# Kernel optimization log

Hardware: AMD Instinct MI355X
Metric: run time of the kernel (lower is better)

## Reference

```python
import jax, jax.numpy as jnp
import numpy as np

B, N, C = 8, 4096, 768
H, HD = 12, 64          # num_heads, head_dim = C // H
M = HD * 2              # rand_feat_dim
LAM = 0.3
NUM_STEP = 5


def setup_inputs() -> dict:
    key = jax.random.key(0)
    k1, k2, k3, k4 = jax.random.split(key, 4)
    x = jax.random.normal(k1, (B, N, C), dtype=jnp.float32)
    Wqkv = jax.random.normal(k2, (C, 2 * C), dtype=jnp.float32) * 0.02
    Wproj = jax.random.normal(k3, (C, C), dtype=jnp.float32) * 0.02
    bproj = jnp.zeros((C,), dtype=jnp.float32)
    rand_matrix = jax.random.normal(k4, (H, HD, M), dtype=jnp.float32)
    return {"x": x, "Wqkv": Wqkv, "Wproj": Wproj, "bproj": bproj,
            "rand_matrix": rand_matrix}


def _soft(z, t):
    # sign(z) * relu(|z| - t): soft-thresholding (ISTA proximal step)
    return jnp.sign(z) * jax.nn.relu(jnp.abs(z) - t)


def reference(x, Wqkv, Wproj, bproj, rand_matrix):
    Bn, Nn, Cn = x.shape
    Hh, hd, m = rand_matrix.shape
    scale = hd ** (-0.5)

    qkv = x @ Wqkv                                   # [B,N,2C]
    q = qkv[..., :Cn].reshape(Bn, Nn, Hh, hd).transpose(0, 2, 1, 3)  # [B,H,N,hd]
    v = qkv[..., Cn:].reshape(Bn, Nn, Hh, hd).transpose(0, 2, 1, 3)  # [B,H,N,hd]

    # random-feature map: exp(q @ proj - ||q||^2 / 2) / sqrt(m)
    qs = q * scale ** 0.5
    rf = jnp.exp(jnp.einsum('bhnd,hdm->bhnm', qs, rand_matrix)
                 - 0.5 * jnp.sum(qs * qs, axis=-1, keepdims=True)) / m ** 0.5
    # F.normalize(p=2, dim=-2): normalize over the sequence axis
    qn = rf / jnp.maximum(jnp.linalg.norm(rf, axis=-2, keepdims=True), 1e-12)

    kk = jnp.einsum('bhnm,bhnp->bhmp', qn, qn)       # [B,H,m,m]
    kv = jnp.einsum('bhnm,bhnd->bhmd', qn, v)        # [B,H,m,hd]

    # Lipschitz bound: max row L1 norm of kk, detached
    L = jax.lax.stop_gradient(
        jnp.max(jnp.sum(jnp.abs(kk), axis=-1), axis=-1))[..., None, None] + 1.0

    # unrolled ISTA soft-thresholding loop
    s = _soft(kv, LAM)
    for _ in range(NUM_STEP):
        s = _soft(s - (kk @ s - kv) / L, LAM / L)

    out = jnp.einsum('bhnm,bhmd->bhnd', qn, s)       # [B,H,N,hd]
    out = out.transpose(0, 2, 1, 3).reshape(Bn, Nn, Cn)
    return out @ Wproj + bproj
```

## Files before the change

kernel.cpp:

```cpp
#include <hip/hip_runtime.h>


typedef __attribute__((ext_vector_type(8))) short bf16x8;
typedef __attribute__((ext_vector_type(4))) float f32x4;

#define GLD16(gptr, lptr)                                                              \
  __builtin_amdgcn_global_load_lds((const __attribute__((address_space(1))) void*)(gptr), \
                                   (__attribute__((address_space(3))) void*)(lptr), 16, 0, 0)

__device__ __forceinline__ unsigned short f2bf(float f) {
  union { float f; unsigned int u; } v; v.f = f;
  unsigned int r = v.u + 0x7fffu + ((v.u >> 16) & 1u);
  return (unsigned short)(r >> 16);
}
__device__ __forceinline__ float bf2f(unsigned short s) {
  union { unsigned int u; float f; } v; v.u = ((unsigned int)s) << 16;
  return v.f;
}
__device__ __forceinline__ float rn_of(float css) {
  return 1.f / fmaxf(sqrtf(css), 1e-12f);
}

template<int ITERS>
__device__ __forceinline__ void gemm256_core(
    const unsigned short* __restrict__ A,
    const unsigned short* __restrict__ B,
    int ldk,
    f32x4 (&acc)[8][4],
    unsigned short* smem) {
  const int tid = threadIdx.x;
  const int lane = tid & 63, wave = tid >> 6;
  const int l16 = lane & 15, quad = lane >> 4;
  const int wr = wave >> 2, wc = wave & 3;
  const int rsw = l16 & 7;

#pragma unroll
  for (int i = 0; i < 8; i++)
#pragma unroll
    for (int j = 0; j < 4; j++)
#pragma unroll
      for (int r = 0; r < 4; r++) acc[i][j][r] = 0.f;

  const int srow0 = tid >> 3, sc0 = ((tid & 7) ^ (srow0 & 7)) << 3;
  const int srow1 = (tid + 512) >> 3, sc1 = ((tid & 7) ^ (srow1 & 7)) << 3;
  const int dstw = wave * 512;

  auto stageA = [&](int T, int h) {
    const unsigned short* g = A + (long)(h * 128) * ldk + T * 64;
    unsigned short* d = smem + (T & 1) * 32768 + h * 8192 + dstw;
    GLD16(g + (long)srow0 * ldk + sc0, d);
    GLD16(g + (long)srow1 * ldk + sc1, d + 4096);
  };
  auto stageB = [&](int T, int h) {
    const unsigned short* g = B + (long)(h * 128) * ldk + T * 64;
    unsigned short* d = smem + (T & 1) * 32768 + 16384 + h * 8192 + dstw;
    GLD16(g + (long)srow0 * ldk + sc0, d);
    GLD16(g + (long)srow1 * ldk + sc1, d + 4096);
  };

  bf16x8 af[4][2], bn[4][2];

  auto rdA_ks = [&](int b, int mh, int ks) {
    const unsigned short* p = smem + b * 32768 + wr * 8192 + (mh * 64 + l16) * 64;
#pragma unroll
    for (int ii = 0; ii < 4; ii++)
      af[ii][ks] = *(const bf16x8*)(p + ii * 1024 + (((ks * 4 + quad) ^ rsw) << 3));
  };
  auto rdB_ks = [&](int b, int ks) {
    const unsigned short* p = smem + b * 32768 + 16384 + (wc >> 1) * 8192 +
                              ((wc & 1) * 64 + l16) * 64;
#pragma unroll
    for (int jj = 0; jj < 4; jj++)
      bn[jj][ks] = *(const bf16x8*)(p + jj * 1024 + (((ks * 4 + quad) ^ rsw) << 3));
  };

  auto mma16 = [&](int mh, int ks) {
    __builtin_amdgcn_s_setprio(1);
#pragma unroll
    for (int ii = 0; ii < 4; ii++)
#pragma unroll
      for (int jj = 0; jj < 4; jj++)
        acc[mh * 4 + ii][jj] = __builtin_amdgcn_mfma_f32_16x16x32_bf16(
            af[ii][ks], bn[jj][ks], acc[mh * 4 + ii][jj], 0, 0, 0);
    __builtin_amdgcn_s_setprio(0);
  };

#define FENCE asm volatile("" ::: "memory")
#define SGB __builtin_amdgcn_sched_barrier(0)
#define LGKM(n) asm volatile("s_waitcnt lgkmcnt(" #n ")" ::: "memory")

  stageA(0, 0); stageA(0, 1); stageB(0, 0); stageB(0, 1);
  stageB(1, 0); stageB(1, 1);
  asm volatile("s_waitcnt vmcnt(4)" ::: "memory");
  __builtin_amdgcn_s_barrier();

#pragma unroll 1
  for (int i = 0; i < ITERS; i++) {
    const int u = 2 * i;
    const bool more = (i + 1 < ITERS);
    stageA(u + 1, 0);
    rdB_ks(0, 0); rdA_ks(0, 0, 0);
    SGB;
    rdB_ks(0, 1); rdA_ks(0, 0, 1);
    FENCE; __builtin_amdgcn_s_barrier();
    LGKM(8); SGB;
    mma16(0, 0);
    LGKM(0); SGB;
    mma16(0, 1);
    FENCE; __builtin_amdgcn_s_barrier();
    stageA(u + 1, 1);
    if (more) stageB(u + 2, 0);
    rdA_ks(0, 1, 0);
    SGB;
    rdA_ks(0, 1, 1);
    FENCE; __builtin_amdgcn_s_barrier();
    LGKM(4); SGB;
    mma16(1, 0);
    LGKM(0); SGB;
    mma16(1, 1);
    if (more) { asm volatile("s_waitcnt vmcnt(2)" ::: "memory"); }
    else      { asm volatile("s_waitcnt vmcnt(0)" ::: "memory"); }
    FENCE; __builtin_amdgcn_s_barrier();
    if (more) { stageB(u + 2, 1); stageA(u + 2, 0); stageA(u + 2, 1); }
    rdB_ks(1, 0); rdA_ks(1, 0, 0);
    SGB;
    rdB_ks(1, 1); rdA_ks(1, 0, 1);
    FENCE; __builtin_amdgcn_s_barrier();
    LGKM(8); SGB;
    mma16(0, 0);
    LGKM(0); SGB;
    mma16(0, 1);
    FENCE; __builtin_amdgcn_s_barrier();
    if (more) { stageB(u + 3, 0); stageB(u + 3, 1); }
    rdA_ks(1, 1, 0);
    SGB;
    rdA_ks(1, 1, 1);
    FENCE; __builtin_amdgcn_s_barrier();
    LGKM(4); SGB;
    mma16(1, 0);
    LGKM(0); SGB;
    mma16(1, 1);
    if (more) { asm volatile("s_waitcnt vmcnt(4)" ::: "memory"); }
    FENCE; __builtin_amdgcn_s_barrier();
  }
#undef FENCE
#undef SGB
#undef LGKM
}

template<int NT>
__device__ __forceinline__ void gemm128x256_core(
    const unsigned short* __restrict__ A,
    const unsigned short* __restrict__ B,
    int ldk,
    f32x4 (&acc)[4][4],
    unsigned short* smem) {
  const int tid = threadIdx.x;
  const int lane = tid & 63, wave = tid >> 6;
  const int l16 = lane & 15, quad = lane >> 4;
  const int wr = wave >> 2, wc = wave & 3;
  const int rsw = l16 & 7;

#pragma unroll
  for (int m = 0; m < 4; m++)
#pragma unroll
    for (int n = 0; n < 4; n++)
#pragma unroll
      for (int r = 0; r < 4; r++) acc[m][n][r] = 0.f;

  const int srow0 = tid >> 3, sc0 = ((tid & 7) ^ (srow0 & 7)) << 3;
  const int srow1 = (tid + 512) >> 3, sc1 = ((tid & 7) ^ (srow1 & 7)) << 3;
  const int dstw = wave * 512;

  auto stage = [&](int T) {
    unsigned short* d = smem + (T & 1) * 24576;
    const unsigned short* gA = A + T * 64;
    const unsigned short* gB = B + T * 64;
    GLD16(gA + (long)srow0 * ldk + sc0, d + dstw);
    GLD16(gA + (long)srow1 * ldk + sc1, d + 4096 + dstw);
    GLD16(gB + (long)srow0 * ldk + sc0, d + 8192 + dstw);
    GLD16(gB + (long)srow1 * ldk + sc1, d + 8192 + 4096 + dstw);
    GLD16(gB + (long)(srow0 + 128) * ldk + sc0, d + 16384 + dstw);
    GLD16(gB + (long)(srow1 + 128) * ldk + sc1, d + 16384 + 4096 + dstw);
  };

  bf16x8 af[4][2], bn[4][2];

  auto rdA_ks = [&](int b, int ks) {
    const unsigned short* p = smem + b * 24576 + (wr * 64 + l16) * 64;
#pragma unroll
    for (int m = 0; m < 4; m++)
      af[m][ks] = *(const bf16x8*)(p + m * 1024 + (((ks * 4 + quad) ^ rsw) << 3));
  };
  auto rdB_ks = [&](int b, int ks) {
    const unsigned short* p = smem + b * 24576 + 8192 + (wc * 64 + l16) * 64;
#pragma unroll
    for (int n = 0; n < 4; n++)
      bn[n][ks] = *(const bf16x8*)(p + n * 1024 + (((ks * 4 + quad) ^ rsw) << 3));
  };

  auto mma16 = [&](int ks) {
    __builtin_amdgcn_s_setprio(1);
#pragma unroll
    for (int m = 0; m < 4; m++)
#pragma unroll
      for (int n = 0; n < 4; n++)
        acc[m][n] = __builtin_amdgcn_mfma_f32_16x16x32_bf16(
            af[m][ks], bn[n][ks], acc[m][n], 0, 0, 0);
    __builtin_amdgcn_s_setprio(0);
  };

#define FENCE asm volatile("" ::: "memory")
#define SGB __builtin_amdgcn_sched_barrier(0)
#define LGKM(n) asm volatile("s_waitcnt lgkmcnt(" #n ")" ::: "memory")

  stage(0); stage(1);
  asm volatile("s_waitcnt vmcnt(6)" ::: "memory");
  __builtin_amdgcn_s_barrier();

#pragma unroll 1
  for (int t = 0; t < NT; t++) {
    const int b = t & 1;
    rdA_ks(b, 0); rdB_ks(b, 0);
    SGB;
    rdA_ks(b, 1); rdB_ks(b, 1);
    LGKM(8); SGB;
    mma16(0);
    LGKM(0); SGB;
    mma16(1);
    FENCE; __builtin_amdgcn_s_barrier();
    if (t + 2 < NT) stage(t + 2);
    if (t + 1 < NT) {
      if (t + 2 < NT) { asm volatile("s_waitcnt vmcnt(6)" ::: "memory"); }
      else            { asm volatile("s_waitcnt vmcnt(0)" ::: "memory"); }
      FENCE; __builtin_amdgcn_s_barrier();
    }
  }
#undef FENCE
#undef SGB
#undef LGKM
}

__global__ __launch_bounds__(256) void k_convert_bf16(const float* __restrict__ in,
                                                      unsigned short* __restrict__ out, long n4) {
  long i = (long)blockIdx.x * 256 + threadIdx.x;
  if (i < n4) {
    float4 v = ((const float4*)in)[i];
    unsigned short o[4] = {f2bf(v.x), f2bf(v.y), f2bf(v.z), f2bf(v.w)};
    ((uint2*)out)[i] = *(uint2*)o;
  }
}

__global__ __launch_bounds__(256) void k_transpose_tiled(const float* __restrict__ in,
                                                         unsigned short* __restrict__ out,
                                                         int R, int C, float scale) {
  __shared__ float t[32][33];
  const float* ib = in + (long)blockIdx.z * R * C;
  unsigned short* ob = out + (long)blockIdx.z * R * C;
  int c0 = blockIdx.x * 32, r0 = blockIdx.y * 32;
  int tx = threadIdx.x & 31, ty = threadIdx.x >> 5;
#pragma unroll
  for (int k = 0; k < 32; k += 8)
    t[ty + k][tx] = ib[(long)(r0 + ty + k) * C + c0 + tx];
  __syncthreads();
#pragma unroll
  for (int k = 0; k < 32; k += 8)
    ob[(long)(c0 + ty + k) * R + r0 + tx] = f2bf(t[tx][ty + k] * scale);
}

__global__ __launch_bounds__(512, 2) void k_gemm_qkv256(const unsigned short* __restrict__ xbf,
                                                        const unsigned short* __restrict__ wqkvT,
                                                        unsigned short* __restrict__ q,
                                                        unsigned short* __restrict__ vT) {
  __shared__ __align__(16) unsigned short smem[65536];
  f32x4 acc[8][4];
  const int L = blockIdx.x;
  const int xcd = L & 7, slot = L >> 3;
  const int rt = xcd * 16 + slot / 6;
  const int ct = slot % 6;
  gemm256_core<6>(xbf + (long)rt * 256 * 768, wqkvT + (long)ct * 256 * 768, 768, acc, smem);

  const int tid = threadIdx.x, lane = tid & 63, wave = tid >> 6;
  const int l16 = lane & 15, quad = lane >> 4;
  const int wr = wave >> 2, wc = wave & 3;
  const int b = rt >> 4;
  const int nbase = (rt & 15) * 256;
  if (ct < 3) {
#pragma unroll
    for (int i = 0; i < 8; i++)
#pragma unroll
      for (int j = 0; j < 4; j++) {
        int col = ct * 256 + wc * 64 + j * 16 + l16;
        int h = col >> 6, d = col & 63;
#pragma unroll
        for (int r = 0; r < 4; r++) {
          int n = nbase + wr * 128 + i * 16 + quad * 4 + r;
          q[((long)(b * 12 + h) * 4096 + n) * 64 + d] = f2bf(acc[i][j][r]);
        }
      }
  } else {
    unsigned short* pool = smem;
    for (int hh = 0; hh < 2; hh++) {
      __syncthreads();
      if (wr == hh) {
#pragma unroll
        for (int i = 0; i < 8; i++)
#pragma unroll
          for (int j = 0; j < 4; j++)
#pragma unroll
            for (int r = 0; r < 4; r++)
              pool[(wc * 64 + j * 16 + l16) * 136 + i * 16 + quad * 4 + r] = f2bf(acc[i][j][r]);
      }
      __syncthreads();
#pragma unroll
      for (int it = 0; it < 8; it++) {
        int chunk = it * 512 + tid;
        int col = chunk >> 4, ng = chunk & 15;
        uint4 val = *(const uint4*)&pool[col * 136 + ng * 8];
        int vcol = (ct - 3) * 256 + col;
        int h = vcol >> 6, d = vcol & 63;
        long n = nbase + hh * 128 + ng * 8;
        *(uint4*)&vT[((long)(b * 12 + h) * 64 + d) * 4096 + n] = val;
      }
    }
  }
}

__global__ __launch_bounds__(256) void k_gemm_rf(const unsigned short* __restrict__ q,
                                                 const unsigned short* __restrict__ rmT,
                                                 unsigned short* __restrict__ qnT,
                                                 float* __restrict__ colss) {
  __shared__ __align__(16) unsigned short smem[16384];
  __shared__ float hnp[256];
  __shared__ float css[128];
  unsigned short* Asm = smem;
  unsigned short* Bsm = smem + 8192;
  unsigned short* pool = smem;
  f32x4 acc[4][4];
  const int nt = blockIdx.x, bh = blockIdx.y, h = bh % 12;
  const int tid = threadIdx.x, lane = tid & 63, wave = tid >> 6;
  const int l16 = lane & 15, quad = lane >> 4;
  const int wm = (wave >> 1) * 64, wn = (wave & 1) * 64;
  const int fsw = (l16 >> 1) & 3;
  const unsigned short* Aq = q + ((long)bh * 4096 + nt * 128) * 64;
  const unsigned short* Brm = rmT + (long)h * 8192;

#pragma unroll
  for (int c = 0; c < 4; c++) {
    int chunk = c * 256 + tid;
    int row = chunk >> 3, ko8 = chunk & 7;
    int kc = ko8 >> 2;
    int c2s = (ko8 & 3) ^ ((row >> 1) & 3);
    *(uint4*)(Asm + kc * 4096 + row * 32 + c2s * 8) = *(const uint4*)(Aq + (long)row * 64 + ko8 * 8);
    *(uint4*)(Bsm + kc * 4096 + row * 32 + c2s * 8) = *(const uint4*)(Brm + (long)row * 64 + ko8 * 8);
  }
  for (int i = tid; i < 128; i += 256) css[i] = 0.f;
  __syncthreads();
  {
    const unsigned short* ap = Asm + (tid & 1) * 4096 + (tid >> 1) * 32;
    float ssum = 0.f;
#pragma unroll
    for (int e = 0; e < 32; e++) { float f = bf2f(ap[e]); ssum += f * f; }
    hnp[tid] = ssum;
  }
#pragma unroll
  for (int i = 0; i < 4; i++)
#pragma unroll
    for (int j = 0; j < 4; j++)
#pragma unroll
      for (int r = 0; r < 4; r++) acc[i][j][r] = 0.f;
#pragma unroll
  for (int kc = 0; kc < 2; kc++) {
    bf16x8 af[4], bfr[4];
#pragma unroll
    for (int i = 0; i < 4; i++)
      af[i] = *(const bf16x8*)(Asm + kc * 4096 + (wm + i * 16 + l16) * 32 + ((quad ^ fsw) * 8));
#pragma unroll
    for (int j = 0; j < 4; j++)
      bfr[j] = *(const bf16x8*)(Bsm + kc * 4096 + (wn + j * 16 + l16) * 32 + ((quad ^ fsw) * 8));
#pragma unroll
    for (int i = 0; i < 4; i++)
#pragma unroll
      for (int j = 0; j < 4; j++)
        acc[i][j] = __builtin_amdgcn_mfma_f32_16x16x32_bf16(af[i], bfr[j], acc[i][j], 0, 0, 0);
  }
  __syncthreads();
  float hnv[4][4];
#pragma unroll
  for (int i = 0; i < 4; i++)
#pragma unroll
    for (int r = 0; r < 4; r++) {
      int row = wm + i * 16 + quad * 4 + r;
      hnv[i][r] = 0.0625f * (hnp[2 * row] + hnp[2 * row + 1]);
    }
#pragma unroll
  for (int j = 0; j < 4; j++) {
    int col = wn + j * 16 + l16;
    float cp = 0.f;
#pragma unroll
    for (int i = 0; i < 4; i++)
#pragma unroll
      for (int r = 0; r < 4; r++) {
        float v = __expf(acc[i][j][r] - hnv[i][r]) * 0.08838834764831845f;
        acc[i][j][r] = v;
        cp += v * v;
      }
    atomicAdd(&css[col], cp);
  }
  __syncthreads();
  for (int i = tid; i < 128; i += 256) atomicAdd(&colss[bh * 128 + i], css[i]);
  for (int hh = 0; hh < 2; hh++) {
    __syncthreads();
    if ((wave >> 1) == hh) {
#pragma unroll
      for (int i = 0; i < 4; i++)
#pragma unroll
        for (int j = 0; j < 4; j++)
#pragma unroll
          for (int r = 0; r < 4; r++)
            pool[(i * 16 + quad * 4 + r) * 134 + wn + j * 16 + l16] = f2bf(acc[i][j][r]);
    }
    __syncthreads();
#pragma unroll
    for (int c = 0; c < 4; c++) {
      int chunk = tid + c * 256;
      int m = chunk >> 3, nj = (chunk & 7) * 8;
      unsigned short o[8];
#pragma unroll
      for (int e = 0; e < 8; e++) o[e] = pool[(nj + e) * 134 + m];
      *(uint4*)&qnT[((long)bh * 128 + m) * 4096 + nt * 128 + hh * 64 + nj] = *(uint4*)o;
    }
  }
}

__global__ __launch_bounds__(256) void k_gemm_kkkv(const unsigned short* __restrict__ qnT,
                                                   const unsigned short* __restrict__ vT,
                                                   const float* __restrict__ colss,
                                                   unsigned short* __restrict__ kkp) {
  __shared__ __align__(16) unsigned short As[128 * 32], Bs[64 * 32];
  f32x4 acc[4][6];
  const int ks = blockIdx.x, bh = blockIdx.y;
  const unsigned short* A = qnT + (long)bh * 128 * 4096 + ks * 512;
  const unsigned short* B1 = vT + (long)bh * 64 * 4096 + ks * 512;
  const int tid = threadIdx.x, lane = tid & 63, wave = tid >> 6;
  const int l16 = lane & 15, quad = lane >> 4;
  const int wm = (wave >> 1) * 64, wn = (wave & 1) * 96;
  const int arow = tid >> 2;
  const int akos = (((tid & 3) ^ ((arow >> 1) & 3)) << 3);
  const int fsw = (l16 >> 1) & 3;
#pragma unroll
  for (int i = 0; i < 4; i++)
#pragma unroll
    for (int j = 0; j < 6; j++)
#pragma unroll
      for (int r = 0; r < 4; r++) acc[i][j][r] = 0.f;
  for (int k0 = 0; k0 < 512; k0 += 32) {
    __syncthreads();
    GLD16(A + (long)arow * 4096 + k0 + akos, As + wave * 512);
    GLD16(A + (long)(arow + 64) * 4096 + k0 + akos, As + 2048 + wave * 512);
    GLD16(B1 + (long)arow * 4096 + k0 + akos, Bs + wave * 512);
    __syncthreads();
    bf16x8 af[4], bfr[6];
#pragma unroll
    for (int i = 0; i < 4; i++)
      af[i] = *(const bf16x8*)(As + (wm + i * 16 + l16) * 32 + ((quad ^ fsw) * 8));
#pragma unroll
    for (int j = 0; j < 6; j++) {
      int row = wn + j * 16 + l16;
      const unsigned short* rp = (row < 128) ? (As + row * 32) : (Bs + (row - 128) * 32);
      bfr[j] = *(const bf16x8*)(rp + ((quad ^ fsw) * 8));
    }
#pragma unroll
    for (int i = 0; i < 4; i++)
#pragma unroll
      for (int j = 0; j < 6; j++)
        acc[i][j] = __builtin_amdgcn_mfma_f32_16x16x32_bf16(af[i], bfr[j], acc[i][j], 0, 0, 0);
  }
  unsigned short* dst = kkp + ((long)ks * 96 + bh) * 24576;
  float rnr[4][4];
#pragma unroll
  for (int i = 0; i < 4; i++)
#pragma unroll
    for (int r = 0; r < 4; r++)
      rnr[i][r] = rn_of(colss[bh * 128 + wm + i * 16 + quad * 4 + r]);
#pragma unroll
  for (int j = 0; j < 6; j++) {
    int col = wn + j * 16 + l16;
    float rnc = (col < 128) ? rn_of(colss[bh * 128 + col]) : 1.f;
#pragma unroll
    for (int i = 0; i < 4; i++)
#pragma unroll
      for (int r = 0; r < 4; r++) {
        int row = wm + i * 16 + quad * 4 + r;
        dst[row * 192 + col] = f2bf(acc[i][j][r] * rnr[i][r] * rnc);
      }
  }
}

__global__ __launch_bounds__(256) void k_red(const unsigned short* __restrict__ kkp,
                                             unsigned short* __restrict__ kkred,
                                             float* __restrict__ kvred) {
  const int g = blockIdx.x, bh = blockIdx.y;
  const int tid = threadIdx.x;
  const unsigned short* base = kkp + (long)bh * 24576 + (long)(g * 32) * 192;
#pragma unroll
  for (int c = 0; c < 3; c++) {
    int idx = c * 256 + tid;
    int m = idx / 24, c8 = idx % 24;
    float f[8] = {0.f, 0.f, 0.f, 0.f, 0.f, 0.f, 0.f, 0.f};
#pragma unroll
    for (int ks = 0; ks < 8; ks++) {
      union { uint4 u; unsigned short s[8]; } u;
      u.u = *(const uint4*)(base + (long)ks * 2359296 + m * 192 + c8 * 8);
#pragma unroll
      for (int e = 0; e < 8; e++) f[e] += bf2f(u.s[e]);
    }
    long row = (long)bh * 128 + g * 32 + m;
    if (c8 < 16) {
      unsigned short o[8];
#pragma unroll
      for (int e = 0; e < 8; e++) o[e] = f2bf(f[e]);
      *(uint4*)&kkred[row * 128 + c8 * 8] = *(uint4*)o;
    } else {
      *(float4*)&kvred[row * 64 + (c8 - 16) * 8] = make_float4(f[0], f[1], f[2], f[3]);
      *(float4*)&kvred[row * 64 + (c8 - 16) * 8 + 4] = make_float4(f[4], f[5], f[6], f[7]);
    }
  }
}

__global__ __launch_bounds__(256) void k_ista2(const unsigned short* __restrict__ kkred,
                                               const float* __restrict__ kvred,
                                               const float* __restrict__ colss,
                                               unsigned short* __restrict__ sT) {
  __shared__ __align__(16) unsigned short kks[128 * 144];
  __shared__ __align__(16) unsigned short ssT[64 * 144];
  __shared__ float kvs[128 * 64];
  __shared__ float red[128];
  __shared__ float rns[128];
  const int tid = threadIdx.x, lane = tid & 63, wave = tid >> 6;
  const int l16 = lane & 15, quad = lane >> 4;
  const int wm = (wave >> 1) * 64, wn = (wave & 1) * 32;
  const int bh = blockIdx.x;
  for (int idx = tid; idx < 2048; idx += 256) {
    int m = idx >> 4, c8 = idx & 15;
    uint4 v = *(const uint4*)(kkred + ((long)bh * 128 + m) * 128 + c8 * 8);
    *(uint4*)&kks[m * 144 + c8 * 8] = v;
  }
  for (int idx = tid; idx < 2048; idx += 256) {
    int m = idx >> 4, c4 = idx & 15;
    float4 v = *(const float4*)(kvred + ((long)bh * 128 + m) * 64 + c4 * 4);
    *(float4*)&kvs[m * 64 + c4 * 4] = v;
  }
  __syncthreads();
  float kv[4][2][4];
#pragma unroll
  for (int i = 0; i < 4; i++)
#pragma unroll
    for (int j = 0; j < 2; j++)
#pragma unroll
      for (int r = 0; r < 4; r++) {
        int m = wm + i * 16 + quad * 4 + r, d = wn + j * 16 + l16;
        kv[i][j][r] = kvs[m * 64 + d];
      }
  if (tid < 128) {
    float rs = 0.f;
    const unsigned short* rp = kks + tid * 144;
    for (int p = 0; p < 128; p++) rs += fabsf(bf2f(rp[p]));
    red[tid] = rs;
    rns[tid] = rn_of(colss[bh * 128 + tid]);
  }
  __syncthreads();
  for (int o = 64; o > 0; o >>= 1) {
    if (tid < o) red[tid] = fmaxf(red[tid], red[tid + o]);
    __syncthreads();
  }
  const float L = red[0] + 1.f;
  const float invL = 1.f / L;
  const float lamL = 0.3f * invL;
  float sreg[4][2][4];
#pragma unroll
  for (int i = 0; i < 4; i++)
#pragma unroll
    for (int j = 0; j < 2; j++)
#pragma unroll
      for (int r = 0; r < 4; r++) {
        float z = kv[i][j][r];
        float az = fabsf(z) - 0.3f;
        float s = az > 0.f ? copysignf(az, z) : 0.f;
        sreg[i][j][r] = s;
        ssT[(wn + j * 16 + l16) * 144 + wm + i * 16 + quad * 4 + r] = f2bf(s);
      }
  for (int step = 0; step < 5; step++) {
    __syncthreads();
    f32x4 acc[4][2];
#pragma unroll
    for (int i = 0; i < 4; i++)
#pragma unroll
      for (int j = 0; j < 2; j++)
#pragma unroll
        for (int r = 0; r < 4; r++) acc[i][j][r] = 0.f;
#pragma unroll
    for (int kc = 0; kc < 4; kc++) {
      bf16x8 af[4], bfj[2];
#pragma unroll
      for (int i = 0; i < 4; i++)
        af[i] = *(const bf16x8*)(kks + (wm + i * 16 + l16) * 144 + kc * 32 + quad * 8);
#pragma unroll
      for (int j = 0; j < 2; j++)
        bfj[j] = *(const bf16x8*)(ssT + (wn + j * 16 + l16) * 144 + kc * 32 + quad * 8);
#pragma unroll
      for (int i = 0; i < 4; i++)
#pragma unroll
        for (int j = 0; j < 2; j++)
          acc[i][j] = __builtin_amdgcn_mfma_f32_16x16x32_bf16(af[i], bfj[j], acc[i][j], 0, 0, 0);
    }
    __syncthreads();
#pragma unroll
    for (int i = 0; i < 4; i++)
#pragma unroll
      for (int j = 0; j < 2; j++)
#pragma unroll
        for (int r = 0; r < 4; r++) {
          float z = sreg[i][j][r] - (acc[i][j][r] - kv[i][j][r]) * invL;
          float az = fabsf(z) - lamL;
          float s = az > 0.f ? copysignf(az, z) : 0.f;
          sreg[i][j][r] = s;
          ssT[(wn + j * 16 + l16) * 144 + wm + i * 16 + quad * 4 + r] = f2bf(s);
        }
  }
#pragma unroll
  for (int i = 0; i < 4; i++)
#pragma unroll
    for (int j = 0; j < 2; j++)
#pragma unroll
      for (int r = 0; r < 4; r++) {
        int m = wm + i * 16 + quad * 4 + r, d = wn + j * 16 + l16;
        sT[(long)bh * 8192 + d * 128 + m] = f2bf(sreg[i][j][r] * rns[m]);
      }
}

__global__ __launch_bounds__(256) void k_gemm_attn(const unsigned short* __restrict__ qnT,
                                                   const unsigned short* __restrict__ sT,
                                                   unsigned short* __restrict__ attn) {
  __shared__ __align__(16) unsigned short As2[4352];
  __shared__ __align__(16) unsigned short Bs[64 * 32];
  f32x4 acc[4][2];
  const int nt = blockIdx.x, bh = blockIdx.y;
  const int b = bh / 12, h = bh % 12;
  const int tid = threadIdx.x, lane = tid & 63, wave = tid >> 6;
  const int l16 = lane & 15, quad = lane >> 4;
  const int wm = (wave >> 1) * 64, wn = (wave & 1) * 32;
  const int fsw = (l16 >> 1) & 3;
#pragma unroll
  for (int i = 0; i < 4; i++)
#pragma unroll
    for (int j = 0; j < 2; j++)
#pragma unroll
      for (int r = 0; r < 4; r++) acc[i][j][r] = 0.f;
  for (int k0 = 0; k0 < 128; k0 += 32) {
    __syncthreads();
#pragma unroll
    for (int it = 0; it < 3; it++) {
      if (it < 2 || tid < 32) {
        int c = it * 256 + tid;
        int p = (c * 241) >> 12;
        int nh = c - p * 17;
        int k = ((p & 7) << 2) + (p >> 3);
        int n8 = (nh < 16 ? nh : 15) << 3;
        const unsigned short* gp = qnT + ((long)bh * 128 + k0 + k) * 4096 + nt * 128 + n8;
        GLD16(gp, As2 + (it * 256 + wave * 64) * 8);
      }
    }
    {
      int dd = tid >> 2;
      int ko = (((tid & 3) ^ ((dd >> 1) & 3)) * 8);
      const unsigned short* gp = sT + ((long)bh * 64 + dd) * 128 + k0 + ko;
      GLD16(gp, Bs + wave * 512);
    }
    __syncthreads();
    bf16x8 af[4], bfr[2];
#pragma unroll
    for (int i = 0; i < 4; i++) {
      union { bf16x8 v; unsigned short s[8]; } u;
#pragma unroll
      for (int e = 0; e < 8; e++) {
        int p = ((e & 3) << 3) + (quad << 1) + (e >> 2);
        u.s[e] = As2[p * 136 + wm + i * 16 + l16];
      }
      af[i] = u.v;
    }
#pragma unroll
    for (int j = 0; j < 2; j++)
      bfr[j] = *(const bf16x8*)&Bs[(wn + j * 16 + l16) * 32 + ((quad ^ fsw) * 8)];
#pragma unroll
    for (int i = 0; i < 4; i++)
#pragma unroll
      for (int j = 0; j < 2; j++)
        acc[i][j] = __builtin_amdgcn_mfma_f32_16x16x32_bf16(af[i], bfr[j], acc[i][j], 0, 0, 0);
  }
#pragma unroll
  for (int i = 0; i < 4; i++)
#pragma unroll
    for (int j = 0; j < 2; j++)
#pragma unroll
      for (int r = 0; r < 4; r++) {
        int n = nt * 128 + wm + i * 16 + quad * 4 + r;
        int dd = wn + j * 16 + l16;
        attn[((long)b * 4096 + n) * 768 + h * 64 + dd] = f2bf(acc[i][j][r]);
      }
}

__global__ __launch_bounds__(512, 2) void k_gemm_proj128(const unsigned short* __restrict__ attn,
                                                         const unsigned short* __restrict__ wprojT,
                                                         const float* __restrict__ bias,
                                                         float* __restrict__ out) {
  __shared__ __align__(16) unsigned short smem[49152];
  f32x4 acc[4][4];
  const int L = blockIdx.x;
  const int xcd = L & 7, slot = L >> 3;
  const int rt = xcd * 32 + slot / 3;
  const int ct = slot % 3;
  gemm128x256_core<12>(attn + (long)rt * 128 * 768, wprojT + (long)ct * 256 * 768, 768,
                       acc, smem);
  const int tid = threadIdx.x, lane = tid & 63, wave = tid >> 6;
  const int l16 = lane & 15, quad = lane >> 4;
  const int wr = wave >> 2, wc = wave & 3;
  const long row0 = (long)rt * 128 + wr * 64;
#pragma unroll
  for (int m = 0; m < 4; m++)
#pragma unroll
    for (int n = 0; n < 4; n++) {
      int col = ct * 256 + wc * 64 + n * 16 + l16;
      float bv = bias[col];
#pragma unroll
      for (int r = 0; r < 4; r++) {
        long row = row0 + m * 16 + quad * 4 + r;
        out[row * 768 + col] = acc[m][n][r] + bv;
      }
    }
}

extern "C" void kernel_launch(void* const* d_in, const int* in_sizes, int n_in,
                              void* d_out, int out_size, void* d_ws, size_t ws_size,
                              hipStream_t stream) {
  const float* x = (const float*)d_in[0];
  const float* Wqkv = (const float*)d_in[1];
  const float* Wproj = (const float*)d_in[2];
  const float* bproj = (const float*)d_in[3];
  const float* rm = (const float*)d_in[4];
  float* out = (float*)d_out;

  size_t o = 0;
  char* wsb = (char*)d_ws;
  auto take = [&](size_t b) { char* p = wsb + o; o += b; return p; };
  unsigned short* wqkvT = (unsigned short*)take(2359296);
  unsigned short* wprojT = (unsigned short*)take(1179648);
  unsigned short* rmT = (unsigned short*)take(196608);
  unsigned short* q = (unsigned short*)take(50331648);
  unsigned short* vT = (unsigned short*)take(50331648);
  float* colss = (float*)take(49152);
  unsigned short* sT = (unsigned short*)take(1572864);
  if (ws_size < o) return;

  unsigned short* xbf = (unsigned short*)d_out;
  unsigned short* qnT = (unsigned short*)d_out;
  unsigned short* kkp = q;
  unsigned short* attnbf = q;
  unsigned short* kkred = vT;
  float* kvred = (float*)(vT + 1572864);

  hipMemsetAsync(colss, 0, 49152, stream);

  k_convert_bf16<<<24576, 256, 0, stream>>>(x, xbf, 6291456L);
  k_transpose_tiled<<<dim3(48, 24, 1), 256, 0, stream>>>(Wqkv, wqkvT, 768, 1536, 1.0f);
  k_transpose_tiled<<<dim3(24, 24, 1), 256, 0, stream>>>(Wproj, wprojT, 768, 768, 1.0f);
  k_transpose_tiled<<<dim3(4, 2, 12), 256, 0, stream>>>(rm, rmT, 64, 128, 0.3535533905932738f);
  k_gemm_qkv256<<<768, 512, 0, stream>>>(xbf, wqkvT, q, vT);
  k_gemm_rf<<<dim3(32, 96), 256, 0, stream>>>(q, rmT, qnT, colss);
  k_gemm_kkkv<<<dim3(8, 96), 256, 0, stream>>>(qnT, vT, colss, kkp);
  k_red<<<dim3(4, 96), 256, 0, stream>>>(kkp, kkred, kvred);
  k_ista2<<<96, 256, 0, stream>>>(kkred, kvred, colss, sT);
  k_gemm_attn<<<dim3(32, 96), 256, 0, stream>>>(qnT, sT, attnbf);
  k_gemm_proj128<<<768, 512, 0, stream>>>(attnbf, wprojT, bproj, out);
}
```

Measured before the change: 450.5 us.

## Merge preprocessing launches into one kernel and split ISTA across head-dim halves

Folds the bf16 conversion of x, the three weight transposes and the colss zeroing into a single k_pre launch, replacing one memset and four separate launches. It also splits the ISTA kernel so each block handles 32 of the 64 head-dim columns, doubling the grid from 96 to 192 blocks. The intent is to cut launch and serialization overhead and to occupy more CUs in the small ISTA stage. The cost is that kk is loaded and its Lipschitz reduction recomputed redundantly in both halves.

```diff
diff --git a/kernel.cpp b/kernel.cpp
--- a/kernel.cpp
+++ b/kernel.cpp
@@ -241,31 +241,53 @@
 #undef LGKM
 }
 
-__global__ __launch_bounds__(256) void k_convert_bf16(const float* __restrict__ in,
-                                                      unsigned short* __restrict__ out, long n4) {
-  long i = (long)blockIdx.x * 256 + threadIdx.x;
-  if (i < n4) {
-    float4 v = ((const float4*)in)[i];
+__global__ __launch_bounds__(256) void k_pre(const float* __restrict__ x,
+                                             unsigned short* __restrict__ xbf,
+                                             const float* __restrict__ Wqkv,
+                                             unsigned short* __restrict__ wqkvT,
+                                             const float* __restrict__ Wproj,
+                                             unsigned short* __restrict__ wprojT,
+                                             const float* __restrict__ rm,
+                                             unsigned short* __restrict__ rmT,
+                                             float* __restrict__ colss) {
+  __shared__ float t[32][33];
+  const int bid = blockIdx.x, tid = threadIdx.x;
+  if (bid < 24576) {
+    long i = (long)bid * 256 + tid;
+    float4 v = ((const float4*)x)[i];
     unsigned short o[4] = {f2bf(v.x), f2bf(v.y), f2bf(v.z), f2bf(v.w)};
-    ((uint2*)out)[i] = *(uint2*)o;
-  }
-}
-
-__global__ __launch_bounds__(256) void k_transpose_tiled(const float* __restrict__ in,
-                                                         unsigned short* __restrict__ out,
-                                                         int R, int C, float scale) {
-  __shared__ float t[32][33];
-  const float* ib = in + (long)blockIdx.z * R * C;
-  unsigned short* ob = out + (long)blockIdx.z * R * C;
-  int c0 = blockIdx.x * 32, r0 = blockIdx.y * 32;
-  int tx = threadIdx.x & 31, ty = threadIdx.x >> 5;
+    ((uint2*)xbf)[i] = *(uint2*)o;
+    return;
+  }
+  int b2 = bid - 24576;
+  const float* in; unsigned short* out; int R, C, c0, r0; float scale;
+  if (b2 < 1152) {
+    in = Wqkv; out = wqkvT; R = 768; C = 1536;
+    c0 = (b2 % 48) * 32; r0 = (b2 / 48) * 32; scale = 1.f;
+  } else if (b2 < 1152 + 576) {
+    b2 -= 1152;
+    in = Wproj; out = wprojT; R = 768; C = 768;
+    c0 = (b2 % 24) * 32; r0 = (b2 / 24) * 32; scale = 1.f;
+  } else if (b2 < 1152 + 576 + 96) {
+    b2 -= 1152 + 576;
+    int z = b2 / 8;
+    in = rm + (long)z * 8192; out = rmT + (long)z * 8192;
+    R = 64; C = 128;
+    c0 = (b2 % 4) * 32; r0 = ((b2 / 4) & 1) * 32;
+    scale = 0.3535533905932738f;
+  } else {
+    b2 -= 1152 + 576 + 96;
+    colss[b2 * 256 + tid] = 0.f;
+    return;
+  }
+  int tx = tid & 31, ty = tid >> 5;
 #pragma unroll
   for (int k = 0; k < 32; k += 8)
-    t[ty + k][tx] = ib[(long)(r0 + ty + k) * C + c0 + tx];
+    t[ty + k][tx] = in[(long)(r0 + ty + k) * C + c0 + tx];
   __syncthreads();
 #pragma unroll
   for (int k = 0; k < 32; k += 8)
-    ob[(long)(c0 + ty + k) * R + r0 + tx] = f2bf(t[tx][ty + k] * scale);
+    out[(long)(c0 + ty + k) * R + r0 + tx] = f2bf(t[tx][ty + k] * scale);
 }
 
 __global__ __launch_bounds__(512, 2) void k_gemm_qkv256(const unsigned short* __restrict__ xbf,
@@ -533,35 +555,33 @@
                                                const float* __restrict__ colss,
                                                unsigned short* __restrict__ sT) {
   __shared__ __align__(16) unsigned short kks[128 * 144];
-  __shared__ __align__(16) unsigned short ssT[64 * 144];
-  __shared__ float kvs[128 * 64];
+  __shared__ __align__(16) unsigned short ssT[32 * 144];
+  __shared__ float kvs[128 * 32];
   __shared__ float red[128];
   __shared__ float rns[128];
   const int tid = threadIdx.x, lane = tid & 63, wave = tid >> 6;
   const int l16 = lane & 15, quad = lane >> 4;
-  const int wm = (wave >> 1) * 64, wn = (wave & 1) * 32;
-  const int bh = blockIdx.x;
+  const int wm = (wave >> 1) * 64, wn = (wave & 1) * 16;
+  const int bh = blockIdx.x >> 1, d0 = (blockIdx.x & 1) * 32;
   for (int idx = tid; idx < 2048; idx += 256) {
     int m = idx >> 4, c8 = idx & 15;
     uint4 v = *(const uint4*)(kkred + ((long)bh * 128 + m) * 128 + c8 * 8);
     *(uint4*)&kks[m * 144 + c8 * 8] = v;
   }
-  for (int idx = tid; idx < 2048; idx += 256) {
-    int m = idx >> 4, c4 = idx & 15;
-    float4 v = *(const float4*)(kvred + ((long)bh * 128 + m) * 64 + c4 * 4);
-    *(float4*)&kvs[m * 64 + c4 * 4] = v;
+  for (int idx = tid; idx < 1024; idx += 256) {
+    int m = idx >> 3, c4 = idx & 7;
+    float4 v = *(const float4*)(kvred + ((long)bh * 128 + m) * 64 + d0 + c4 * 4);
+    *(float4*)&kvs[m * 32 + c4 * 4] = v;
   }
   __syncthreads();
-  float kv[4][2][4];
-#pragma unroll
-  for (int i = 0; i < 4; i++)
-#pragma unroll
-    for (int j = 0; j < 2; j++)
-#pragma unroll
-      for (int r = 0; r < 4; r++) {
-        int m = wm + i * 16 + quad * 4 + r, d = wn + j * 16 + l16;
-        kv[i][j][r] = kvs[m * 64 + d];
-      }
+  float kv[4][4];
+#pragma unroll
+  for (int i = 0; i < 4; i++)
+#pragma unroll
+    for (int r = 0; r < 4; r++) {
+      int m = wm + i * 16 + quad * 4 + r, dl = wn + l16;
+      kv[i][r] = kvs[m * 32 + dl];
+    }
   if (tid < 128) {
     float rs = 0.f;
     const unsigned short* rp = kks + tid * 144;
@@ -577,66 +597,54 @@
   const float L = red[0] + 1.f;
   const float invL = 1.f / L;
   const float lamL = 0.3f * invL;
-  float sreg[4][2][4];
-#pragma unroll
-  for (int i = 0; i < 4; i++)
-#pragma unroll
-    for (int j = 0; j < 2; j++)
-#pragma unroll
-      for (int r = 0; r < 4; r++) {
-        float z = kv[i][j][r];
-        float az = fabsf(z) - 0.3f;
-        float s = az > 0.f ? copysignf(az, z) : 0.f;
-        sreg[i][j][r] = s;
-        ssT[(wn + j * 16 + l16) * 144 + wm + i * 16 + quad * 4 + r] = f2bf(s);
-      }
+  float sreg[4][4];
+#pragma unroll
+  for (int i = 0; i < 4; i++)
+#pragma unroll
+    for (int r = 0; r < 4; r++) {
+      float z = kv[i][r];
+      float az = fabsf(z) - 0.3f;
+      float s = az > 0.f ? copysignf(az, z) : 0.f;
+      sreg[i][r] = s;
+      ssT[(wn + l16) * 144 + wm + i * 16 + quad * 4 + r] = f2bf(s);
+    }
   for (int step = 0; step < 5; step++) {
     __syncthreads();
-    f32x4 acc[4][2];
-#pragma unroll
-    for (int i = 0; i < 4; i++)
-#pragma unroll
-      for (int j = 0; j < 2; j++)
-#pragma unroll
-        for (int r = 0; r < 4; r++) acc[i][j][r] = 0.f;
+    f32x4 acc[4];
+#pragma unroll
+    for (int i = 0; i < 4; i++)
+#pragma unroll
+      for (int r = 0; r < 4; r++) acc[i][r] = 0.f;
 #pragma unroll
     for (int kc = 0; kc < 4; kc++) {
-      bf16x8 af[4], bfj[2];
+      bf16x8 af[4], bfj;
 #pragma unroll
       for (int i = 0; i < 4; i++)
         af[i] = *(const bf16x8*)(kks + (wm + i * 16 + l16) * 144 + kc * 32 + quad * 8);
-#pragma unroll
-      for (int j = 0; j < 2; j++)
-        bfj[j] = *(const bf16x8*)(ssT + (wn + j * 16 + l16) * 144 + kc * 32 + quad * 8);
+      bfj = *(const bf16x8*)(ssT + (wn + l16) * 144 + kc * 32 + quad * 8);
 #pragma unroll
       for (int i = 0; i < 4; i++)
-#pragma unroll
-        for (int j = 0; j < 2; j++)
-          acc[i][j] = __builtin_amdgcn_mfma_f32_16x16x32_bf16(af[i], bfj[j], acc[i][j], 0, 0, 0);
-    }
-    __syncthreads();
-#pragma unroll
-    for (int i = 0; i < 4; i++)
-#pragma unroll
-      for (int j = 0; j < 2; j++)
-#pragma unroll
-        for (int r = 0; r < 4; r++) {
-          float z = sreg[i][j][r] - (acc[i][j][r] - kv[i][j][r]) * invL;
-          float az = fabsf(z) - lamL;
-          float s = az > 0.f ? copysignf(az, z) : 0.f;
-          sreg[i][j][r] = s;
-          ssT[(wn + j * 16 + l16) * 144 + wm + i * 16 + quad * 4 + r] = f2bf(s);
-        }
-  }
-#pragma unroll
-  for (int i = 0; i < 4; i++)
-#pragma unroll
-    for (int j = 0; j < 2; j++)
+        acc[i] = __builtin_amdgcn_mfma_f32_16x16x32_bf16(af[i], bfj, acc[i], 0, 0, 0);
+    }
+    __syncthreads();
+#pragma unroll
+    for (int i = 0; i < 4; i++)
 #pragma unroll
       for (int r = 0; r < 4; r++) {
-        int m = wm + i * 16 + quad * 4 + r, d = wn + j * 16 + l16;
-        sT[(long)bh * 8192 + d * 128 + m] = f2bf(sreg[i][j][r] * rns[m]);
-      }
+        float z = sreg[i][r] - (acc[i][r] - kv[i][r]) * invL;
+        float az = fabsf(z) - lamL;
+        float s = az > 0.f ? copysignf(az, z) : 0.f;
+        sreg[i][r] = s;
+        ssT[(wn + l16) * 144 + wm + i * 16 + quad * 4 + r] = f2bf(s);
+      }
+  }
+#pragma unroll
+  for (int i = 0; i < 4; i++)
+#pragma unroll
+    for (int r = 0; r < 4; r++) {
+      int m = wm + i * 16 + quad * 4 + r, d = d0 + wn + l16;
+      sT[(long)bh * 8192 + d * 128 + m] = f2bf(sreg[i][r] * rns[m]);
+    }
 }
 
 __global__ __launch_bounds__(256) void k_gemm_attn(const unsigned short* __restrict__ qnT,
@@ -769,17 +777,12 @@
   unsigned short* kkred = vT;
   float* kvred = (float*)(vT + 1572864);
 
-  hipMemsetAsync(colss, 0, 49152, stream);
-
-  k_convert_bf16<<<24576, 256, 0, stream>>>(x, xbf, 6291456L);
-  k_transpose_tiled<<<dim3(48, 24, 1), 256, 0, stream>>>(Wqkv, wqkvT, 768, 1536, 1.0f);
-  k_transpose_tiled<<<dim3(24, 24, 1), 256, 0, stream>>>(Wproj, wprojT, 768, 768, 1.0f);
-  k_transpose_tiled<<<dim3(4, 2, 12), 256, 0, stream>>>(rm, rmT, 64, 128, 0.3535533905932738f);
+  k_pre<<<26448, 256, 0, stream>>>(x, xbf, Wqkv, wqkvT, Wproj, wprojT, rm, rmT, colss);
   k_gemm_qkv256<<<768, 512, 0, stream>>>(xbf, wqkvT, q, vT);
   k_gemm_rf<<<dim3(32, 96), 256, 0, stream>>>(q, rmT, qnT, colss);
   k_gemm_kkkv<<<dim3(8, 96), 256, 0, stream>>>(qnT, vT, colss, kkp);
   k_red<<<dim3(4, 96), 256, 0, stream>>>(kkp, kkred, kvred);
-  k_ista2<<<96, 256, 0, stream>>>(kkred, kvred, colss, sT);
+  k_ista2<<<192, 256, 0, stream>>>(kkred, kvred, colss, sT);
   k_gemm_attn<<<dim3(32, 96), 256, 0, stream>>>(qnT, sT, attnbf);
   k_gemm_proj128<<<768, 512, 0, stream>>>(attnbf, wprojT, bproj, out);
 }
```

Measured after the change: 441.7 us. 1.02x faster.
